# Performance work log

Hardware: AMD Instinct MI355X
Metric: run time of the kernel (lower is better)

The kernel has to match this reference:

```python
import jax, jax.numpy as jnp
import numpy as np

THETA = 40.0


def setup_inputs() -> dict:
    key = jax.random.key(0)
    k1, k2 = jax.random.split(key)
    B, C, H, W = 4, 19, 192, 192
    mask = jax.random.normal(k1, (B, C, H, W), dtype=jnp.float32)
    edge = jax.random.uniform(k2, (B, 1, H, W), dtype=jnp.float32)
    return {"mask": mask, "edge": edge, "iter": 3}


def _criss_cross_attention(edge):
    # edge: [B,1,H,W] -> attention logits over K = H + W - 1 criss-cross positions
    e = jax.nn.relu(edge)
    max_edge = e.max()
    hc = jnp.cumsum(e, axis=2)[:, 0]  # [B,H,W] column integral image
    wc = jnp.cumsum(e, axis=3)[:, 0]  # [B,H,W] row integral image
    B, H, W = hc.shape
    # column part: weight[b,t,i,j] = |hc[b,t,j] - hc[b,i,j]|, t in [0,H)
    w_col = jnp.abs(hc[:, :, None, :] - hc[:, None, :, :])  # [B,H,H,W] (b,t,i,j)
    # row part over all columns s: |wc[b,i,s] - wc[b,i,j]|
    wct = wc.transpose(0, 2, 1)  # [B,W(s),H(i)]
    w_row_full = jnp.abs(wct[:, :, :, None] - wc[:, None, :, :])  # [B,W,H,W] (b,s,i,j)
    # drop s == j (self column, already counted in column part): W-1 entries
    t = jnp.arange(W - 1)[:, None]
    j = jnp.arange(W)[None, :]
    idx = t + (t >= j).astype(t.dtype)  # [W-1, W]: source column for slot t at pixel column j
    w_row = jnp.take_along_axis(w_row_full, idx[None, :, None, :], axis=1)  # [B,W-1,H,W]
    logits = -THETA * (jnp.concatenate([w_col, w_row], axis=1) - max_edge)  # [B,H+W-1,H,W]
    attn = jax.nn.softmax(logits, axis=1)
    a_col = attn[:, :H]  # [B,H,H,W]
    a_row = attn[:, H:]  # [B,W-1,H,W]
    # scatter row attention back to full [B,W,H,W] (zero at s==j) for a dense einsum
    attn_full = jnp.zeros((B, W, H, W), attn.dtype).at[:, idx, :, j].set(
        a_row.transpose(1, 3, 0, 2)
    )
    return a_col, attn_full


def reference(mask, edge, iter):
    a_col, a_row_full = _criss_cross_attention(edge)
    feat = mask  # [B,C,H,W]
    for _ in range(iter):
        out_c = jnp.einsum('btij,bctj->bcij', a_col, feat)       # column gather
        out_r = jnp.einsum('bsij,bcis->bcij', a_row_full, feat)  # row gather
        feat = out_c + out_r
    return feat
```

## Files before the change

kernel.cpp:

```cpp
#include <hip/hip_runtime.h>

#define B 4
#define C 19
#define H 192
#define W 192
#define HW (H * W)
#define THETA_LOG2E 57.70780163555855f

#define CSEGS 8
#define CSR 24

template<bool DENOM>
__global__ __launch_bounds__(512) void k_col(const float* __restrict__ fin,
                                             const float* __restrict__ edge,
                                             float* __restrict__ csum,
                                             float* __restrict__ dcolg) {
    int blk = blockIdx.x;
    int jt = blk % 3;
    int bc = blk / 3;
    int b = bc / C;
    int c = bc % C;
    int jl = threadIdx.x & 63, seg = threadIdx.x >> 6;
    int j = jt * 64 + jl;
    int i0 = seg * CSR;

    const float* ep = edge + ((size_t)b * H + i0) * W + j;
    const float* fp = fin + ((size_t)bc * H + i0) * W + j;
    float* op = csum + ((size_t)bc * H + i0) * W + j;

    float dr[CSR + 1], fr[CSR];
    #pragma unroll
    for (int r = 0; r < CSR; ++r) {
        float e = ep[r * W];
        dr[r] = exp2f(-THETA_LOG2E * fmaxf(e, 0.f));
        fr[r] = fp[r * W];
    }
    if (seg < CSEGS - 1) {
        float e = ep[CSR * W];
        dr[CSR] = exp2f(-THETA_LOG2E * fmaxf(e, 0.f));
    } else {
        dr[CSR] = 0.f;
    }

    __shared__ float sPf[CSEGS][64], sQf[CSEGS][64], sPb[CSEGS][64], sQb[CSEGS][64];

    float Pf = 1.f, Qf = 0.f, Pb = 1.f, Qb = 0.f;
    #pragma unroll
    for (int r = 0; r < CSR; ++r) { Qf = Qf * dr[r] + fr[r]; Pf *= dr[r]; }
    #pragma unroll
    for (int r = CSR - 1; r >= 0; --r) { Qb = Qb * dr[r + 1] + fr[r]; Pb *= dr[r + 1]; }
    sPf[seg][jl] = Pf; sQf[seg][jl] = Qf;
    sPb[seg][jl] = Pb; sQb[seg][jl] = Qb;
    __syncthreads();
    if (seg == 0) {
        float P = sPf[0][jl], Q = sQf[0][jl];
        for (int s2 = 1; s2 < CSEGS; ++s2) {
            float Pc = sPf[s2][jl], Qc = sQf[s2][jl];
            Q = Q * Pc + Qc; P = P * Pc;
            sPf[s2][jl] = P; sQf[s2][jl] = Q;
        }
    } else if (seg == 1) {
        float P = sPb[CSEGS - 1][jl], Q = sQb[CSEGS - 1][jl];
        for (int s2 = CSEGS - 2; s2 >= 0; --s2) {
            float Pc = sPb[s2][jl], Qc = sQb[s2][jl];
            Q = Q * Pc + Qc; P = P * Pc;
            sPb[s2][jl] = P; sQb[s2][jl] = Q;
        }
    }
    __syncthreads();
    float z = (seg > 0) ? sQf[seg - 1][jl] : 0.f;
    float s = (seg < CSEGS - 1) ? sQb[seg + 1][jl] : 0.f;
    float zarr[CSR];
    #pragma unroll
    for (int r = 0; r < CSR; ++r) { z = z * dr[r] + fr[r]; zarr[r] = z; }
    #pragma unroll
    for (int r = CSR - 1; r >= 0; --r) {
        s = s * dr[r + 1] + fr[r];
        op[r * W] = zarr[r] + s - fr[r];
    }

    if (DENOM && c == 0) {
        float Pf2 = 1.f, Qf2 = 0.f, Pb2 = 1.f, Qb2 = 0.f;
        #pragma unroll
        for (int r = 0; r < CSR; ++r) { Qf2 = Qf2 * dr[r] + 1.f; Pf2 *= dr[r]; }
        #pragma unroll
        for (int r = CSR - 1; r >= 0; --r) { Qb2 = Qb2 * dr[r + 1] + 1.f; Pb2 *= dr[r + 1]; }
        __syncthreads();
        sPf[seg][jl] = Pf2; sQf[seg][jl] = Qf2;
        sPb[seg][jl] = Pb2; sQb[seg][jl] = Qb2;
        __syncthreads();
        if (seg == 0) {
            float P = sPf[0][jl], Q = sQf[0][jl];
            for (int s2 = 1; s2 < CSEGS; ++s2) {
                float Pc = sPf[s2][jl], Qc = sQf[s2][jl];
                Q = Q * Pc + Qc; P = P * Pc;
                sPf[s2][jl] = P; sQf[s2][jl] = Q;
            }
        } else if (seg == 1) {
            float P = sPb[CSEGS - 1][jl], Q = sQb[CSEGS - 1][jl];
            for (int s2 = CSEGS - 2; s2 >= 0; --s2) {
                float Pc = sPb[s2][jl], Qc = sQb[s2][jl];
                Q = Q * Pc + Qc; P = P * Pc;
                sPb[s2][jl] = P; sQb[s2][jl] = Q;
            }
        }
        __syncthreads();
        float zu = (seg > 0) ? sQf[seg - 1][jl] : 0.f;
        float su = (seg < CSEGS - 1) ? sQb[seg + 1][jl] : 0.f;
        float* dop = dcolg + ((size_t)b * H + i0) * W + j;
        #pragma unroll
        for (int r = 0; r < CSR; ++r) { zu = zu * dr[r] + 1.f; zarr[r] = zu; }
        #pragma unroll
        for (int r = CSR - 1; r >= 0; --r) {
            su = su * dr[r + 1] + 1.f;
            dop[r * W] = zarr[r] + su - 1.f;
        }
    }
}

template<bool FIRST>
__global__ __launch_bounds__(256) void k_row(const float* fin,
                                             float* fout,
                                             const float* __restrict__ edge,
                                             const float* __restrict__ csum,
                                             const float* __restrict__ dcolg,
                                             float* __restrict__ rDg) {
    int wid = (blockIdx.x * 256 + threadIdx.x) >> 6;
    int lane = threadIdx.x & 63;
    int i = wid % H;
    int c = (wid / H) % C;
    int b = wid / (H * C);
    const size_t rb = ((size_t)(b * C + c) * H + i) * W;
    const int db = (b * H + i) * W;
    const int s0 = 3 * lane;

    float e0 = edge[db + s0], e1 = edge[db + s0 + 1], e2 = edge[db + s0 + 2];
    float d0 = exp2f(-THETA_LOG2E * fmaxf(e0, 0.f));
    float d1 = exp2f(-THETA_LOG2E * fmaxf(e1, 0.f));
    float d2 = exp2f(-THETA_LOG2E * fmaxf(e2, 0.f));
    float d3 = 0.f;
    if (lane < 63) {
        float e3 = edge[db + s0 + 3];
        d3 = exp2f(-THETA_LOG2E * fmaxf(e3, 0.f));
    }
    float f0 = fin[rb + s0], f1 = fin[rb + s0 + 1], f2 = fin[rb + s0 + 2];

    float P = d0 * d1 * d2;
    float Q = (f0 * d1 + f1) * d2 + f2;
    #pragma unroll
    for (int off = 1; off < 64; off <<= 1) {
        float Pp = __shfl_up(P, off);
        float Qp = __shfl_up(Q, off);
        if (lane >= off) { Q = Qp * P + Q; P = Pp * P; }
    }
    float zin = __shfl_up(Q, 1);
    if (lane == 0) zin = 0.f;
    float zA = zin * d0 + f0;
    float zB = zA * d1 + f1;
    float zC = zB * d2 + f2;

    float Pb = d3 * d2 * d1;
    float Qb = (f2 * d2 + f1) * d1 + f0;
    #pragma unroll
    for (int off = 1; off < 64; off <<= 1) {
        float Pp = __shfl_down(Pb, off);
        float Qp = __shfl_down(Qb, off);
        if (lane < 64 - off) { Qb = Qp * Pb + Qb; Pb = Pp * Pb; }
    }
    float sin_ = __shfl_down(Qb, 1);
    if (lane == 63) sin_ = 0.f;
    float sC = sin_ * d3 + f2;
    float sB = sC * d2 + f1;
    float sA = sB * d1 + f0;

    float rd0, rd1, rd2;
    if (FIRST) {
        float Pu = d0 * d1 * d2;
        float Qu = d1 * d2 + d2 + 1.f;
        #pragma unroll
        for (int off = 1; off < 64; off <<= 1) {
            float Pp = __shfl_up(Pu, off);
            float Qp = __shfl_up(Qu, off);
            if (lane >= off) { Qu = Qp * Pu + Qu; Pu = Pp * Pu; }
        }
        float zuin = __shfl_up(Qu, 1);
        if (lane == 0) zuin = 0.f;
        float zuA = zuin * d0 + 1.f;
        float zuB = zuA * d1 + 1.f;
        float zuC = zuB * d2 + 1.f;

        float Pub = d3 * d2 * d1;
        float Qub = d2 * d1 + d1 + 1.f;
        #pragma unroll
        for (int off = 1; off < 64; off <<= 1) {
            float Pp = __shfl_down(Pub, off);
            float Qp = __shfl_down(Qub, off);
            if (lane < 64 - off) { Qub = Qp * Pub + Qub; Pub = Pp * Pub; }
        }
        float suin = __shfl_down(Qub, 1);
        if (lane == 63) suin = 0.f;
        float suC = suin * d3 + 1.f;
        float suB = suC * d2 + 1.f;
        float suA = suB * d1 + 1.f;

        rd0 = 1.f / (dcolg[db + s0]     + zuA + suA - 2.f);
        rd1 = 1.f / (dcolg[db + s0 + 1] + zuB + suB - 2.f);
        rd2 = 1.f / (dcolg[db + s0 + 2] + zuC + suC - 2.f);
        if (c == 0) {
            rDg[db + s0]     = rd0;
            rDg[db + s0 + 1] = rd1;
            rDg[db + s0 + 2] = rd2;
        }
    } else {
        rd0 = rDg[db + s0];
        rd1 = rDg[db + s0 + 1];
        rd2 = rDg[db + s0 + 2];
    }

    float cs0 = csum[rb + s0], cs1 = csum[rb + s0 + 1], cs2 = csum[rb + s0 + 2];
    fout[rb + s0]     = (cs0 + zA + sA - 2.f * f0) * rd0;
    fout[rb + s0 + 1] = (cs1 + zB + sB - 2.f * f1) * rd1;
    fout[rb + s0 + 2] = (cs2 + zC + sC - 2.f * f2) * rd2;
}

extern "C" void kernel_launch(void* const* d_in, const int* in_sizes, int n_in,
                              void* d_out, int out_size, void* d_ws, size_t ws_size,
                              hipStream_t stream) {
    const float* mask = (const float*)d_in[0];
    const float* edge = (const float*)d_in[1];
    float* out = (float*)d_out;

    float* csum = (float*)d_ws;
    float* dcol = csum + (size_t)B * C * HW;
    float* rDg  = dcol + B * HW;

    const int colgrid = B * C * 3;
    const int rowgrid = (B * C * H) / 4;

    k_col<true><<<colgrid, 512, 0, stream>>>(mask, edge, csum, dcol);
    k_row<true><<<rowgrid, 256, 0, stream>>>(mask, out, edge, csum, dcol, rDg);
    k_col<false><<<colgrid, 512, 0, stream>>>(out, edge, csum, nullptr);
    k_row<false><<<rowgrid, 256, 0, stream>>>(out, out, edge, csum, nullptr, rDg);
    k_col<false><<<colgrid, 512, 0, stream>>>(out, edge, csum, nullptr);
    k_row<false><<<rowgrid, 256, 0, stream>>>(out, out, edge, csum, nullptr, rDg);
}
```

Measured before the change: 57.33 us.

## Fuse six column/row launches into one cooperative kernel with grid syncs

Replaces the six separate kernel launches (three column-scan and three row-scan phases) with one cooperative persistent kernel of 228 blocks that runs each phase and separates them with grid.sync(). Each block handles one column tile and loops over eight row-waves per phase. The aim is to remove launch gaps and per-kernel ramp-up and drain between the small phases. The cost is grid-barrier overhead and fixed occupancy, and the old multi-launch path remains as a fallback if the cooperative launch fails.

Result: slower. 218.5 us (+281.0%).

```diff
diff --git a/kernel.cpp b/kernel.cpp
--- a/kernel.cpp
+++ b/kernel.cpp
@@ -1,4 +1,7 @@
 #include <hip/hip_runtime.h>
+#include <hip/hip_cooperative_groups.h>
+
+namespace cg = cooperative_groups;
 
 #define B 4
 #define C 19
@@ -9,18 +12,23 @@
 
 #define CSEGS 8
 #define CSR 24
+#define NBLK 228
+#define NTHR 512
+#define NWAVES (NBLK * 8)
+#define NROWS (B * C * H)
 
 template<bool DENOM>
-__global__ __launch_bounds__(512) void k_col(const float* __restrict__ fin,
-                                             const float* __restrict__ edge,
-                                             float* __restrict__ csum,
-                                             float* __restrict__ dcolg) {
-    int blk = blockIdx.x;
+__device__ __forceinline__ void col_phase(const float* __restrict__ fin,
+                                          const float* __restrict__ edge,
+                                          float* __restrict__ csum,
+                                          float* __restrict__ dcolg,
+                                          float* sPf, float* sQf, float* sPb, float* sQb,
+                                          int blk, int t) {
     int jt = blk % 3;
     int bc = blk / 3;
     int b = bc / C;
     int c = bc % C;
-    int jl = threadIdx.x & 63, seg = threadIdx.x >> 6;
+    int jl = t & 63, seg = t >> 6;
     int j = jt * 64 + jl;
     int i0 = seg * CSR;
 
@@ -31,45 +39,37 @@
     float dr[CSR + 1], fr[CSR];
     #pragma unroll
     for (int r = 0; r < CSR; ++r) {
-        float e = ep[r * W];
-        dr[r] = exp2f(-THETA_LOG2E * fmaxf(e, 0.f));
+        dr[r] = exp2f(-THETA_LOG2E * fmaxf(ep[r * W], 0.f));
         fr[r] = fp[r * W];
     }
-    if (seg < CSEGS - 1) {
-        float e = ep[CSR * W];
-        dr[CSR] = exp2f(-THETA_LOG2E * fmaxf(e, 0.f));
-    } else {
-        dr[CSR] = 0.f;
-    }
-
-    __shared__ float sPf[CSEGS][64], sQf[CSEGS][64], sPb[CSEGS][64], sQb[CSEGS][64];
+    dr[CSR] = (seg < CSEGS - 1) ? exp2f(-THETA_LOG2E * fmaxf(ep[CSR * W], 0.f)) : 0.f;
 
     float Pf = 1.f, Qf = 0.f, Pb = 1.f, Qb = 0.f;
     #pragma unroll
     for (int r = 0; r < CSR; ++r) { Qf = Qf * dr[r] + fr[r]; Pf *= dr[r]; }
     #pragma unroll
     for (int r = CSR - 1; r >= 0; --r) { Qb = Qb * dr[r + 1] + fr[r]; Pb *= dr[r + 1]; }
-    sPf[seg][jl] = Pf; sQf[seg][jl] = Qf;
-    sPb[seg][jl] = Pb; sQb[seg][jl] = Qb;
+    sPf[seg * 64 + jl] = Pf; sQf[seg * 64 + jl] = Qf;
+    sPb[seg * 64 + jl] = Pb; sQb[seg * 64 + jl] = Qb;
     __syncthreads();
     if (seg == 0) {
-        float P = sPf[0][jl], Q = sQf[0][jl];
+        float P = sPf[jl], Q = sQf[jl];
         for (int s2 = 1; s2 < CSEGS; ++s2) {
-            float Pc = sPf[s2][jl], Qc = sQf[s2][jl];
+            float Pc = sPf[s2 * 64 + jl], Qc = sQf[s2 * 64 + jl];
             Q = Q * Pc + Qc; P = P * Pc;
-            sPf[s2][jl] = P; sQf[s2][jl] = Q;
+            sPf[s2 * 64 + jl] = P; sQf[s2 * 64 + jl] = Q;
         }
     } else if (seg == 1) {
-        float P = sPb[CSEGS - 1][jl], Q = sQb[CSEGS - 1][jl];
+        float P = sPb[(CSEGS - 1) * 64 + jl], Q = sQb[(CSEGS - 1) * 64 + jl];
         for (int s2 = CSEGS - 2; s2 >= 0; --s2) {
-            float Pc = sPb[s2][jl], Qc = sQb[s2][jl];
+            float Pc = sPb[s2 * 64 + jl], Qc = sQb[s2 * 64 + jl];
             Q = Q * Pc + Qc; P = P * Pc;
-            sPb[s2][jl] = P; sQb[s2][jl] = Q;
+            sPb[s2 * 64 + jl] = P; sQb[s2 * 64 + jl] = Q;
         }
     }
     __syncthreads();
-    float z = (seg > 0) ? sQf[seg - 1][jl] : 0.f;
-    float s = (seg < CSEGS - 1) ? sQb[seg + 1][jl] : 0.f;
+    float z = (seg > 0) ? sQf[(seg - 1) * 64 + jl] : 0.f;
+    float s = (seg < CSEGS - 1) ? sQb[(seg + 1) * 64 + jl] : 0.f;
     float zarr[CSR];
     #pragma unroll
     for (int r = 0; r < CSR; ++r) { z = z * dr[r] + fr[r]; zarr[r] = z; }
@@ -86,27 +86,27 @@
         #pragma unroll
         for (int r = CSR - 1; r >= 0; --r) { Qb2 = Qb2 * dr[r + 1] + 1.f; Pb2 *= dr[r + 1]; }
         __syncthreads();
-        sPf[seg][jl] = Pf2; sQf[seg][jl] = Qf2;
-        sPb[seg][jl] = Pb2; sQb[seg][jl] = Qb2;
+        sPf[seg * 64 + jl] = Pf2; sQf[seg * 64 + jl] = Qf2;
+        sPb[seg * 64 + jl] = Pb2; sQb[seg * 64 + jl] = Qb2;
         __syncthreads();
         if (seg == 0) {
-            float P = sPf[0][jl], Q = sQf[0][jl];
+            float P = sPf[jl], Q = sQf[jl];
             for (int s2 = 1; s2 < CSEGS; ++s2) {
-                float Pc = sPf[s2][jl], Qc = sQf[s2][jl];
+                float Pc = sPf[s2 * 64 + jl], Qc = sQf[s2 * 64 + jl];
                 Q = Q * Pc + Qc; P = P * Pc;
-                sPf[s2][jl] = P; sQf[s2][jl] = Q;
+                sPf[s2 * 64 + jl] = P; sQf[s2 * 64 + jl] = Q;
             }
         } else if (seg == 1) {
-            float P = sPb[CSEGS - 1][jl], Q = sQb[CSEGS - 1][jl];
+            float P = sPb[(CSEGS - 1) * 64 + jl], Q = sQb[(CSEGS - 1) * 64 + jl];
             for (int s2 = CSEGS - 2; s2 >= 0; --s2) {
-                float Pc = sPb[s2][jl], Qc = sQb[s2][jl];
+                float Pc = sPb[s2 * 64 + jl], Qc = sQb[s2 * 64 + jl];
                 Q = Q * Pc + Qc; P = P * Pc;
-                sPb[s2][jl] = P; sQb[s2][jl] = Q;
+                sPb[s2 * 64 + jl] = P; sQb[s2 * 64 + jl] = Q;
             }
         }
         __syncthreads();
-        float zu = (seg > 0) ? sQf[seg - 1][jl] : 0.f;
-        float su = (seg < CSEGS - 1) ? sQb[seg + 1][jl] : 0.f;
+        float zu = (seg > 0) ? sQf[(seg - 1) * 64 + jl] : 0.f;
+        float su = (seg < CSEGS - 1) ? sQb[(seg + 1) * 64 + jl] : 0.f;
         float* dop = dcolg + ((size_t)b * H + i0) * W + j;
         #pragma unroll
         for (int r = 0; r < CSR; ++r) { zu = zu * dr[r] + 1.f; zarr[r] = zu; }
@@ -119,17 +119,15 @@
 }
 
 template<bool FIRST>
-__global__ __launch_bounds__(256) void k_row(const float* fin,
-                                             float* fout,
-                                             const float* __restrict__ edge,
-                                             const float* __restrict__ csum,
-                                             const float* __restrict__ dcolg,
-                                             float* __restrict__ rDg) {
-    int wid = (blockIdx.x * 256 + threadIdx.x) >> 6;
-    int lane = threadIdx.x & 63;
-    int i = wid % H;
-    int c = (wid / H) % C;
-    int b = wid / (H * C);
+__device__ __forceinline__ void row_one(int rr, int lane,
+                                        const float* fin, float* fout,
+                                        const float* __restrict__ edge,
+                                        const float* __restrict__ csum,
+                                        const float* __restrict__ dcolg,
+                                        float* __restrict__ rDg) {
+    const int i = rr % H;
+    const int c = (rr / H) % C;
+    const int b = rr / (H * C);
     const size_t rb = ((size_t)(b * C + c) * H + i) * W;
     const int db = (b * H + i) * W;
     const int s0 = 3 * lane;
@@ -223,6 +221,62 @@
     fout[rb + s0 + 2] = (cs2 + zC + sC - 2.f * f2) * rd2;
 }
 
+template<bool FIRST>
+__device__ __forceinline__ void row_phase(const float* fin, float* fout,
+                                          const float* __restrict__ edge,
+                                          const float* __restrict__ csum,
+                                          const float* __restrict__ dcolg,
+                                          float* __restrict__ rDg,
+                                          int blk, int t) {
+    const int wave = t >> 6, lane = t & 63;
+    const int gw = blk * 8 + wave;
+    for (int k = 0; k < 8; ++k)
+        row_one<FIRST>(gw + k * NWAVES, lane, fin, fout, edge, csum, dcolg, rDg);
+}
+
+__global__ __launch_bounds__(NTHR, 2) void k_coop(const float* __restrict__ mask,
+                                                  const float* __restrict__ edge,
+                                                  float* __restrict__ outg,
+                                                  float* __restrict__ csum,
+                                                  float* __restrict__ dcolg,
+                                                  float* __restrict__ rDg) {
+    __shared__ float sPf[CSEGS * 64], sQf[CSEGS * 64], sPb[CSEGS * 64], sQb[CSEGS * 64];
+    cg::grid_group grid = cg::this_grid();
+    const int t = threadIdx.x, blk = blockIdx.x;
+
+    col_phase<true>(mask, edge, csum, dcolg, sPf, sQf, sPb, sQb, blk, t);
+    grid.sync();
+    row_phase<true>(mask, outg, edge, csum, dcolg, rDg, blk, t);
+    grid.sync();
+    col_phase<false>(outg, edge, csum, nullptr, sPf, sQf, sPb, sQb, blk, t);
+    grid.sync();
+    row_phase<false>(outg, outg, edge, csum, nullptr, rDg, blk, t);
+    grid.sync();
+    col_phase<false>(outg, edge, csum, nullptr, sPf, sQf, sPb, sQb, blk, t);
+    grid.sync();
+    row_phase<false>(outg, outg, edge, csum, nullptr, rDg, blk, t);
+}
+
+template<bool DENOM>
+__global__ __launch_bounds__(512) void k_col(const float* __restrict__ fin,
+                                             const float* __restrict__ edge,
+                                             float* __restrict__ csum,
+                                             float* __restrict__ dcolg) {
+    __shared__ float sPf[CSEGS * 64], sQf[CSEGS * 64], sPb[CSEGS * 64], sQb[CSEGS * 64];
+    col_phase<DENOM>(fin, edge, csum, dcolg, sPf, sQf, sPb, sQb, blockIdx.x, threadIdx.x);
+}
+
+template<bool FIRST>
+__global__ __launch_bounds__(256) void k_row(const float* fin, float* fout,
+                                             const float* __restrict__ edge,
+                                             const float* __restrict__ csum,
+                                             const float* __restrict__ dcolg,
+                                             float* __restrict__ rDg) {
+    int wid = (blockIdx.x * 256 + threadIdx.x) >> 6;
+    int lane = threadIdx.x & 63;
+    row_one<FIRST>(wid, lane, fin, fout, edge, csum, dcolg, rDg);
+}
+
 extern "C" void kernel_launch(void* const* d_in, const int* in_sizes, int n_in,
                               void* d_out, int out_size, void* d_ws, size_t ws_size,
                               hipStream_t stream) {
@@ -234,13 +288,19 @@
     float* dcol = csum + (size_t)B * C * HW;
     float* rDg  = dcol + B * HW;
 
-    const int colgrid = B * C * 3;
-    const int rowgrid = (B * C * H) / 4;
-
-    k_col<true><<<colgrid, 512, 0, stream>>>(mask, edge, csum, dcol);
-    k_row<true><<<rowgrid, 256, 0, stream>>>(mask, out, edge, csum, dcol, rDg);
-    k_col<false><<<colgrid, 512, 0, stream>>>(out, edge, csum, nullptr);
-    k_row<false><<<rowgrid, 256, 0, stream>>>(out, out, edge, csum, nullptr, rDg);
-    k_col<false><<<colgrid, 512, 0, stream>>>(out, edge, csum, nullptr);
-    k_row<false><<<rowgrid, 256, 0, stream>>>(out, out, edge, csum, nullptr, rDg);
-}
+    void* args[] = {(void*)&mask, (void*)&edge, (void*)&out,
+                    (void*)&csum, (void*)&dcol, (void*)&rDg};
+    hipError_t err = hipLaunchCooperativeKernel((const void*)k_coop, dim3(NBLK), dim3(NTHR),
+                                                args, 0, stream);
+    if (err != hipSuccess) {
+        (void)hipGetLastError();
+        const int colgrid = B * C * 3;
+        const int rowgrid = (B * C * H) / 4;
+        k_col<true><<<colgrid, 512, 0, stream>>>(mask, edge, csum, dcol);
+        k_row<true><<<rowgrid, 256, 0, stream>>>(mask, out, edge, csum, dcol, rDg);
+        k_col<false><<<colgrid, 512, 0, stream>>>(out, edge, csum, nullptr);
+        k_row<false><<<rowgrid, 256, 0, stream>>>(out, out, edge, csum, nullptr, rDg);
+        k_col<false><<<colgrid, 512, 0, stream>>>(out, edge, csum, nullptr);
+        k_row<false><<<rowgrid, 256, 0, stream>>>(out, out, edge, csum, nullptr, rDg);
+    }
+}
```

## Run column and row passes concurrently per iteration with bf16 partial sums

Applied to the files above, without the earlier changes.

Column and row passes used to run one after the other, with the row pass consuming the column result. They now run as independent block ranges of a single kernel per iteration, both reading the same normalised input. The next iteration rebuilds its input from the stored column and row partial sums plus the column and row denominators, and a final combine kernel writes the output. Partial sums are stored in bf16 to halve intermediate traffic, and there are four launches instead of six. The cost is extra rounding error from bf16 intermediates, plus a reciprocal recomputed on every load.

Result: faster. 50.91 us (-11.2%).

```diff
diff --git a/kernel.cpp b/kernel.cpp
--- a/kernel.cpp
+++ b/kernel.cpp
@@ -9,218 +9,250 @@
 
 #define CSEGS 8
 #define CSR 24
-
-template<bool DENOM>
-__global__ __launch_bounds__(512) void k_col(const float* __restrict__ fin,
-                                             const float* __restrict__ edge,
-                                             float* __restrict__ csum,
-                                             float* __restrict__ dcolg) {
-    int blk = blockIdx.x;
-    int jt = blk % 3;
-    int bc = blk / 3;
-    int b = bc / C;
-    int c = bc % C;
-    int jl = threadIdx.x & 63, seg = threadIdx.x >> 6;
-    int j = jt * 64 + jl;
-    int i0 = seg * CSR;
-
-    const float* ep = edge + ((size_t)b * H + i0) * W + j;
-    const float* fp = fin + ((size_t)bc * H + i0) * W + j;
-    float* op = csum + ((size_t)bc * H + i0) * W + j;
-
-    float dr[CSR + 1], fr[CSR];
-    #pragma unroll
-    for (int r = 0; r < CSR; ++r) {
-        float e = ep[r * W];
-        dr[r] = exp2f(-THETA_LOG2E * fmaxf(e, 0.f));
-        fr[r] = fp[r * W];
-    }
-    if (seg < CSEGS - 1) {
-        float e = ep[CSR * W];
-        dr[CSR] = exp2f(-THETA_LOG2E * fmaxf(e, 0.f));
-    } else {
-        dr[CSR] = 0.f;
-    }
-
-    __shared__ float sPf[CSEGS][64], sQf[CSEGS][64], sPb[CSEGS][64], sQb[CSEGS][64];
-
-    float Pf = 1.f, Qf = 0.f, Pb = 1.f, Qb = 0.f;
-    #pragma unroll
-    for (int r = 0; r < CSR; ++r) { Qf = Qf * dr[r] + fr[r]; Pf *= dr[r]; }
-    #pragma unroll
-    for (int r = CSR - 1; r >= 0; --r) { Qb = Qb * dr[r + 1] + fr[r]; Pb *= dr[r + 1]; }
-    sPf[seg][jl] = Pf; sQf[seg][jl] = Qf;
-    sPb[seg][jl] = Pb; sQb[seg][jl] = Qb;
-    __syncthreads();
-    if (seg == 0) {
-        float P = sPf[0][jl], Q = sQf[0][jl];
-        for (int s2 = 1; s2 < CSEGS; ++s2) {
-            float Pc = sPf[s2][jl], Qc = sQf[s2][jl];
-            Q = Q * Pc + Qc; P = P * Pc;
-            sPf[s2][jl] = P; sQf[s2][jl] = Q;
-        }
-    } else if (seg == 1) {
-        float P = sPb[CSEGS - 1][jl], Q = sQb[CSEGS - 1][jl];
-        for (int s2 = CSEGS - 2; s2 >= 0; --s2) {
-            float Pc = sPb[s2][jl], Qc = sQb[s2][jl];
-            Q = Q * Pc + Qc; P = P * Pc;
-            sPb[s2][jl] = P; sQb[s2][jl] = Q;
-        }
-    }
-    __syncthreads();
-    float z = (seg > 0) ? sQf[seg - 1][jl] : 0.f;
-    float s = (seg < CSEGS - 1) ? sQb[seg + 1][jl] : 0.f;
-    float zarr[CSR];
-    #pragma unroll
-    for (int r = 0; r < CSR; ++r) { z = z * dr[r] + fr[r]; zarr[r] = z; }
-    #pragma unroll
-    for (int r = CSR - 1; r >= 0; --r) {
-        s = s * dr[r + 1] + fr[r];
-        op[r * W] = zarr[r] + s - fr[r];
-    }
-
-    if (DENOM && c == 0) {
-        float Pf2 = 1.f, Qf2 = 0.f, Pb2 = 1.f, Qb2 = 0.f;
-        #pragma unroll
-        for (int r = 0; r < CSR; ++r) { Qf2 = Qf2 * dr[r] + 1.f; Pf2 *= dr[r]; }
-        #pragma unroll
-        for (int r = CSR - 1; r >= 0; --r) { Qb2 = Qb2 * dr[r + 1] + 1.f; Pb2 *= dr[r + 1]; }
-        __syncthreads();
-        sPf[seg][jl] = Pf2; sQf[seg][jl] = Qf2;
-        sPb[seg][jl] = Pb2; sQb[seg][jl] = Qb2;
+#define NCOLB (B * C * 3)
+#define NROWB (B * C * H / 8)
+#define NTHR 512
+
+__device__ __forceinline__ unsigned short f2b(float x) {
+    unsigned u = __float_as_uint(x);
+    u = (u + 0x7FFFu + ((u >> 16) & 1u)) >> 16;
+    return (unsigned short)u;
+}
+__device__ __forceinline__ float b2f(unsigned short h) {
+    return __uint_as_float(((unsigned)h) << 16);
+}
+
+template<bool FIRST>
+__global__ __launch_bounds__(NTHR) void k_iter(const float* __restrict__ mask,
+                                               const float* __restrict__ edge,
+                                               const unsigned short* __restrict__ csin,
+                                               const unsigned short* __restrict__ rsin,
+                                               unsigned short* __restrict__ csout,
+                                               unsigned short* __restrict__ rsout,
+                                               float* __restrict__ dcol,
+                                               float* __restrict__ drow) {
+    const int t = threadIdx.x;
+    if (blockIdx.x < NCOLB) {
+        __shared__ float sPf[CSEGS * 64], sQf[CSEGS * 64], sPb[CSEGS * 64], sQb[CSEGS * 64];
+        int blk = blockIdx.x;
+        int jt = blk % 3, bc = blk / 3, b = bc / C, c = bc % C;
+        int jl = t & 63, seg = t >> 6;
+        int j = jt * 64 + jl, i0 = seg * CSR;
+
+        const float* ep = edge + ((size_t)b * H + i0) * W + j;
+        const size_t fb = ((size_t)bc * H + i0) * W + j;
+        const size_t db = ((size_t)b * H + i0) * W + j;
+
+        float dr[CSR + 1], fr[CSR];
+        #pragma unroll
+        for (int r = 0; r < CSR; ++r) dr[r] = exp2f(-THETA_LOG2E * fmaxf(ep[r * W], 0.f));
+        dr[CSR] = (seg < CSEGS - 1) ? exp2f(-THETA_LOG2E * fmaxf(ep[CSR * W], 0.f)) : 0.f;
+
+        if (FIRST) {
+            #pragma unroll
+            for (int r = 0; r < CSR; ++r) fr[r] = mask[fb + r * W];
+        } else {
+            #pragma unroll
+            for (int r = 0; r < CSR; ++r) {
+                float cs = b2f(csin[fb + r * W]);
+                float rs = b2f(rsin[fb + r * W]);
+                float rd = 1.f / (dcol[db + r * W] + drow[db + r * W] - 1.f);
+                fr[r] = (cs + rs) * rd;
+            }
+        }
+
+        float Pf = 1.f, Qf = 0.f, Pb = 1.f, Qb = 0.f;
+        #pragma unroll
+        for (int r = 0; r < CSR; ++r) { Qf = Qf * dr[r] + fr[r]; Pf *= dr[r]; }
+        #pragma unroll
+        for (int r = CSR - 1; r >= 0; --r) { Qb = Qb * dr[r + 1] + fr[r]; Pb *= dr[r + 1]; }
+        sPf[seg * 64 + jl] = Pf; sQf[seg * 64 + jl] = Qf;
+        sPb[seg * 64 + jl] = Pb; sQb[seg * 64 + jl] = Qb;
         __syncthreads();
         if (seg == 0) {
-            float P = sPf[0][jl], Q = sQf[0][jl];
+            float P = sPf[jl], Q = sQf[jl];
             for (int s2 = 1; s2 < CSEGS; ++s2) {
-                float Pc = sPf[s2][jl], Qc = sQf[s2][jl];
+                float Pc = sPf[s2 * 64 + jl], Qc = sQf[s2 * 64 + jl];
                 Q = Q * Pc + Qc; P = P * Pc;
-                sPf[s2][jl] = P; sQf[s2][jl] = Q;
+                sPf[s2 * 64 + jl] = P; sQf[s2 * 64 + jl] = Q;
             }
         } else if (seg == 1) {
-            float P = sPb[CSEGS - 1][jl], Q = sQb[CSEGS - 1][jl];
+            float P = sPb[(CSEGS - 1) * 64 + jl], Q = sQb[(CSEGS - 1) * 64 + jl];
             for (int s2 = CSEGS - 2; s2 >= 0; --s2) {
-                float Pc = sPb[s2][jl], Qc = sQb[s2][jl];
+                float Pc = sPb[s2 * 64 + jl], Qc = sQb[s2 * 64 + jl];
                 Q = Q * Pc + Qc; P = P * Pc;
-                sPb[s2][jl] = P; sQb[s2][jl] = Q;
+                sPb[s2 * 64 + jl] = P; sQb[s2 * 64 + jl] = Q;
             }
         }
         __syncthreads();
-        float zu = (seg > 0) ? sQf[seg - 1][jl] : 0.f;
-        float su = (seg < CSEGS - 1) ? sQb[seg + 1][jl] : 0.f;
-        float* dop = dcolg + ((size_t)b * H + i0) * W + j;
-        #pragma unroll
-        for (int r = 0; r < CSR; ++r) { zu = zu * dr[r] + 1.f; zarr[r] = zu; }
+        float z = (seg > 0) ? sQf[(seg - 1) * 64 + jl] : 0.f;
+        float s = (seg < CSEGS - 1) ? sQb[(seg + 1) * 64 + jl] : 0.f;
+        float zarr[CSR];
+        #pragma unroll
+        for (int r = 0; r < CSR; ++r) { z = z * dr[r] + fr[r]; zarr[r] = z; }
         #pragma unroll
         for (int r = CSR - 1; r >= 0; --r) {
-            su = su * dr[r + 1] + 1.f;
-            dop[r * W] = zarr[r] + su - 1.f;
+            s = s * dr[r + 1] + fr[r];
+            csout[fb + r * W] = f2b(zarr[r] + s - fr[r]);
+        }
+
+        if (FIRST && c == 0) {
+            float Pf2 = 1.f, Qf2 = 0.f, Pb2 = 1.f, Qb2 = 0.f;
+            #pragma unroll
+            for (int r = 0; r < CSR; ++r) { Qf2 = Qf2 * dr[r] + 1.f; Pf2 *= dr[r]; }
+            #pragma unroll
+            for (int r = CSR - 1; r >= 0; --r) { Qb2 = Qb2 * dr[r + 1] + 1.f; Pb2 *= dr[r + 1]; }
+            __syncthreads();
+            sPf[seg * 64 + jl] = Pf2; sQf[seg * 64 + jl] = Qf2;
+            sPb[seg * 64 + jl] = Pb2; sQb[seg * 64 + jl] = Qb2;
+            __syncthreads();
+            if (seg == 0) {
+                float P = sPf[jl], Q = sQf[jl];
+                for (int s2 = 1; s2 < CSEGS; ++s2) {
+                    float Pc = sPf[s2 * 64 + jl], Qc = sQf[s2 * 64 + jl];
+                    Q = Q * Pc + Qc; P = P * Pc;
+                    sPf[s2 * 64 + jl] = P; sQf[s2 * 64 + jl] = Q;
+                }
+            } else if (seg == 1) {
+                float P = sPb[(CSEGS - 1) * 64 + jl], Q = sQb[(CSEGS - 1) * 64 + jl];
+                for (int s2 = CSEGS - 2; s2 >= 0; --s2) {
+                    float Pc = sPb[s2 * 64 + jl], Qc = sQb[s2 * 64 + jl];
+                    Q = Q * Pc + Qc; P = P * Pc;
+                    sPb[s2 * 64 + jl] = P; sQb[s2 * 64 + jl] = Q;
+                }
+            }
+            __syncthreads();
+            float zu = (seg > 0) ? sQf[(seg - 1) * 64 + jl] : 0.f;
+            float su = (seg < CSEGS - 1) ? sQb[(seg + 1) * 64 + jl] : 0.f;
+            #pragma unroll
+            for (int r = 0; r < CSR; ++r) { zu = zu * dr[r] + 1.f; zarr[r] = zu; }
+            #pragma unroll
+            for (int r = CSR - 1; r >= 0; --r) {
+                su = su * dr[r + 1] + 1.f;
+                dcol[db + r * W] = zarr[r] + su - 1.f;
+            }
+        }
+    } else {
+        int rblk = blockIdx.x - NCOLB;
+        int wave = t >> 6, lane = t & 63;
+        int rr = rblk * 8 + wave;
+        int i = rr % H;
+        int c = (rr / H) % C;
+        int b = rr / (H * C);
+        const size_t rb = ((size_t)(b * C + c) * H + i) * W;
+        const int db = (b * H + i) * W;
+        const int s0 = 3 * lane;
+
+        float e0 = edge[db + s0], e1 = edge[db + s0 + 1], e2 = edge[db + s0 + 2];
+        float d0 = exp2f(-THETA_LOG2E * fmaxf(e0, 0.f));
+        float d1 = exp2f(-THETA_LOG2E * fmaxf(e1, 0.f));
+        float d2 = exp2f(-THETA_LOG2E * fmaxf(e2, 0.f));
+        float d3 = 0.f;
+        if (lane < 63) {
+            float e3 = edge[db + s0 + 3];
+            d3 = exp2f(-THETA_LOG2E * fmaxf(e3, 0.f));
+        }
+
+        float f0, f1, f2;
+        if (FIRST) {
+            f0 = mask[rb + s0]; f1 = mask[rb + s0 + 1]; f2 = mask[rb + s0 + 2];
+        } else {
+            float rd0 = 1.f / (dcol[db + s0]     + drow[db + s0]     - 1.f);
+            float rd1 = 1.f / (dcol[db + s0 + 1] + drow[db + s0 + 1] - 1.f);
+            float rd2 = 1.f / (dcol[db + s0 + 2] + drow[db + s0 + 2] - 1.f);
+            f0 = (b2f(csin[rb + s0])     + b2f(rsin[rb + s0]))     * rd0;
+            f1 = (b2f(csin[rb + s0 + 1]) + b2f(rsin[rb + s0 + 1])) * rd1;
+            f2 = (b2f(csin[rb + s0 + 2]) + b2f(rsin[rb + s0 + 2])) * rd2;
+        }
+
+        float P = d0 * d1 * d2;
+        float Q = (f0 * d1 + f1) * d2 + f2;
+        #pragma unroll
+        for (int off = 1; off < 64; off <<= 1) {
+            float Pp = __shfl_up(P, off);
+            float Qp = __shfl_up(Q, off);
+            if (lane >= off) { Q = Qp * P + Q; P = Pp * P; }
+        }
+        float zin = __shfl_up(Q, 1);
+        if (lane == 0) zin = 0.f;
+        float zA = zin * d0 + f0;
+        float zB = zA * d1 + f1;
+        float zC = zB * d2 + f2;
+
+        float Pb = d3 * d2 * d1;
+        float Qb = (f2 * d2 + f1) * d1 + f0;
+        #pragma unroll
+        for (int off = 1; off < 64; off <<= 1) {
+            float Pp = __shfl_down(Pb, off);
+            float Qp = __shfl_down(Qb, off);
+            if (lane < 64 - off) { Qb = Qp * Pb + Qb; Pb = Pp * Pb; }
+        }
+        float sin_ = __shfl_down(Qb, 1);
+        if (lane == 63) sin_ = 0.f;
+        float sC = sin_ * d3 + f2;
+        float sB = sC * d2 + f1;
+        float sA = sB * d1 + f0;
+
+        rsout[rb + s0]     = f2b(zA + sA - 2.f * f0);
+        rsout[rb + s0 + 1] = f2b(zB + sB - 2.f * f1);
+        rsout[rb + s0 + 2] = f2b(zC + sC - 2.f * f2);
+
+        if (FIRST && c == 0) {
+            float Pu = d0 * d1 * d2;
+            float Qu = d1 * d2 + d2 + 1.f;
+            #pragma unroll
+            for (int off = 1; off < 64; off <<= 1) {
+                float Pp = __shfl_up(Pu, off);
+                float Qp = __shfl_up(Qu, off);
+                if (lane >= off) { Qu = Qp * Pu + Qu; Pu = Pp * Pu; }
+            }
+            float zuin = __shfl_up(Qu, 1);
+            if (lane == 0) zuin = 0.f;
+            float zuA = zuin * d0 + 1.f;
+            float zuB = zuA * d1 + 1.f;
+            float zuC = zuB * d2 + 1.f;
+
+            float Pub = d3 * d2 * d1;
+            float Qub = d2 * d1 + d1 + 1.f;
+            #pragma unroll
+            for (int off = 1; off < 64; off <<= 1) {
+                float Pp = __shfl_down(Pub, off);
+                float Qp = __shfl_down(Qub, off);
+                if (lane < 64 - off) { Qub = Qp * Pub + Qub; Pub = Pp * Pub; }
+            }
+            float suin = __shfl_down(Qub, 1);
+            if (lane == 63) suin = 0.f;
+            float suC = suin * d3 + 1.f;
+            float suB = suC * d2 + 1.f;
+            float suA = suB * d1 + 1.f;
+
+            drow[db + s0]     = zuA + suA - 1.f;
+            drow[db + s0 + 1] = zuB + suB - 1.f;
+            drow[db + s0 + 2] = zuC + suC - 1.f;
         }
     }
 }
 
-template<bool FIRST>
-__global__ __launch_bounds__(256) void k_row(const float* fin,
-                                             float* fout,
-                                             const float* __restrict__ edge,
-                                             const float* __restrict__ csum,
-                                             const float* __restrict__ dcolg,
-                                             float* __restrict__ rDg) {
-    int wid = (blockIdx.x * 256 + threadIdx.x) >> 6;
-    int lane = threadIdx.x & 63;
-    int i = wid % H;
-    int c = (wid / H) % C;
-    int b = wid / (H * C);
-    const size_t rb = ((size_t)(b * C + c) * H + i) * W;
-    const int db = (b * H + i) * W;
-    const int s0 = 3 * lane;
-
-    float e0 = edge[db + s0], e1 = edge[db + s0 + 1], e2 = edge[db + s0 + 2];
-    float d0 = exp2f(-THETA_LOG2E * fmaxf(e0, 0.f));
-    float d1 = exp2f(-THETA_LOG2E * fmaxf(e1, 0.f));
-    float d2 = exp2f(-THETA_LOG2E * fmaxf(e2, 0.f));
-    float d3 = 0.f;
-    if (lane < 63) {
-        float e3 = edge[db + s0 + 3];
-        d3 = exp2f(-THETA_LOG2E * fmaxf(e3, 0.f));
-    }
-    float f0 = fin[rb + s0], f1 = fin[rb + s0 + 1], f2 = fin[rb + s0 + 2];
-
-    float P = d0 * d1 * d2;
-    float Q = (f0 * d1 + f1) * d2 + f2;
-    #pragma unroll
-    for (int off = 1; off < 64; off <<= 1) {
-        float Pp = __shfl_up(P, off);
-        float Qp = __shfl_up(Q, off);
-        if (lane >= off) { Q = Qp * P + Q; P = Pp * P; }
-    }
-    float zin = __shfl_up(Q, 1);
-    if (lane == 0) zin = 0.f;
-    float zA = zin * d0 + f0;
-    float zB = zA * d1 + f1;
-    float zC = zB * d2 + f2;
-
-    float Pb = d3 * d2 * d1;
-    float Qb = (f2 * d2 + f1) * d1 + f0;
-    #pragma unroll
-    for (int off = 1; off < 64; off <<= 1) {
-        float Pp = __shfl_down(Pb, off);
-        float Qp = __shfl_down(Qb, off);
-        if (lane < 64 - off) { Qb = Qp * Pb + Qb; Pb = Pp * Pb; }
-    }
-    float sin_ = __shfl_down(Qb, 1);
-    if (lane == 63) sin_ = 0.f;
-    float sC = sin_ * d3 + f2;
-    float sB = sC * d2 + f1;
-    float sA = sB * d1 + f0;
-
-    float rd0, rd1, rd2;
-    if (FIRST) {
-        float Pu = d0 * d1 * d2;
-        float Qu = d1 * d2 + d2 + 1.f;
-        #pragma unroll
-        for (int off = 1; off < 64; off <<= 1) {
-            float Pp = __shfl_up(Pu, off);
-            float Qp = __shfl_up(Qu, off);
-            if (lane >= off) { Qu = Qp * Pu + Qu; Pu = Pp * Pu; }
-        }
-        float zuin = __shfl_up(Qu, 1);
-        if (lane == 0) zuin = 0.f;
-        float zuA = zuin * d0 + 1.f;
-        float zuB = zuA * d1 + 1.f;
-        float zuC = zuB * d2 + 1.f;
-
-        float Pub = d3 * d2 * d1;
-        float Qub = d2 * d1 + d1 + 1.f;
-        #pragma unroll
-        for (int off = 1; off < 64; off <<= 1) {
-            float Pp = __shfl_down(Pub, off);
-            float Qp = __shfl_down(Qub, off);
-            if (lane < 64 - off) { Qub = Qp * Pub + Qub; Pub = Pp * Pub; }
-        }
-        float suin = __shfl_down(Qub, 1);
-        if (lane == 63) suin = 0.f;
-        float suC = suin * d3 + 1.f;
-        float suB = suC * d2 + 1.f;
-        float suA = suB * d1 + 1.f;
-
-        rd0 = 1.f / (dcolg[db + s0]     + zuA + suA - 2.f);
-        rd1 = 1.f / (dcolg[db + s0 + 1] + zuB + suB - 2.f);
-        rd2 = 1.f / (dcolg[db + s0 + 2] + zuC + suC - 2.f);
-        if (c == 0) {
-            rDg[db + s0]     = rd0;
-            rDg[db + s0 + 1] = rd1;
-            rDg[db + s0 + 2] = rd2;
-        }
-    } else {
-        rd0 = rDg[db + s0];
-        rd1 = rDg[db + s0 + 1];
-        rd2 = rDg[db + s0 + 2];
-    }
-
-    float cs0 = csum[rb + s0], cs1 = csum[rb + s0 + 1], cs2 = csum[rb + s0 + 2];
-    fout[rb + s0]     = (cs0 + zA + sA - 2.f * f0) * rd0;
-    fout[rb + s0 + 1] = (cs1 + zB + sB - 2.f * f1) * rd1;
-    fout[rb + s0 + 2] = (cs2 + zC + sC - 2.f * f2) * rd2;
+__global__ __launch_bounds__(256) void k_comb(const unsigned short* __restrict__ cs,
+                                              const unsigned short* __restrict__ rs,
+                                              const float* __restrict__ dcol,
+                                              const float* __restrict__ drow,
+                                              float* __restrict__ out) {
+    int idx4 = (blockIdx.x * 256 + threadIdx.x) * 4;
+    int bc = idx4 / HW;
+    int rem = idx4 - bc * HW;
+    int b = bc / C;
+    size_t db = (size_t)b * HW + rem;
+    uint2 csu = *(const uint2*)(cs + idx4);
+    uint2 rsu = *(const uint2*)(rs + idx4);
+    float4 dc = *(const float4*)(dcol + db);
+    float4 dw = *(const float4*)(drow + db);
+    float4 o;
+    o.x = (b2f((unsigned short)(csu.x & 0xffff)) + b2f((unsigned short)(rsu.x & 0xffff))) / (dc.x + dw.x - 1.f);
+    o.y = (b2f((unsigned short)(csu.x >> 16))    + b2f((unsigned short)(rsu.x >> 16)))    / (dc.y + dw.y - 1.f);
+    o.z = (b2f((unsigned short)(csu.y & 0xffff)) + b2f((unsigned short)(rsu.y & 0xffff))) / (dc.z + dw.z - 1.f);
+    o.w = (b2f((unsigned short)(csu.y >> 16))    + b2f((unsigned short)(rsu.y >> 16)))    / (dc.w + dw.w - 1.f);
+    *(float4*)(out + idx4) = o;
 }
 
 extern "C" void kernel_launch(void* const* d_in, const int* in_sizes, int n_in,
@@ -230,17 +262,17 @@
     const float* edge = (const float*)d_in[1];
     float* out = (float*)d_out;
 
-    float* csum = (float*)d_ws;
-    float* dcol = csum + (size_t)B * C * HW;
-    float* rDg  = dcol + B * HW;
-
-    const int colgrid = B * C * 3;
-    const int rowgrid = (B * C * H) / 4;
-
-    k_col<true><<<colgrid, 512, 0, stream>>>(mask, edge, csum, dcol);
-    k_row<true><<<rowgrid, 256, 0, stream>>>(mask, out, edge, csum, dcol, rDg);
-    k_col<false><<<colgrid, 512, 0, stream>>>(out, edge, csum, nullptr);
-    k_row<false><<<rowgrid, 256, 0, stream>>>(out, out, edge, csum, nullptr, rDg);
-    k_col<false><<<colgrid, 512, 0, stream>>>(out, edge, csum, nullptr);
-    k_row<false><<<rowgrid, 256, 0, stream>>>(out, out, edge, csum, nullptr, rDg);
-}
+    float* dcol = (float*)d_ws;
+    float* drow = dcol + (size_t)B * HW;
+    unsigned short* csA = (unsigned short*)(drow + (size_t)B * HW);
+    unsigned short* rsA = csA + (size_t)B * C * HW;
+    unsigned short* csB = rsA + (size_t)B * C * HW;
+    unsigned short* rsB = csB + (size_t)B * C * HW;
+
+    const int grid = NCOLB + NROWB;
+
+    k_iter<true><<<grid, NTHR, 0, stream>>>(mask, edge, nullptr, nullptr, csA, rsA, dcol, drow);
+    k_iter<false><<<grid, NTHR, 0, stream>>>(nullptr, edge, csA, rsA, csB, rsB, dcol, drow);
+    k_iter<false><<<grid, NTHR, 0, stream>>>(nullptr, edge, csB, rsB, csA, rsA, dcol, drow);
+    k_comb<<<(B * C * HW) / (4 * 256), 256, 0, stream>>>(csA, rsA, dcol, drow, out);
+}
```
